# Kernel optimization log

Hardware: AMD Instinct MI355X
Metric: run time of the kernel (lower is better)

The kernel has to match this reference:

```python
import jax, jax.numpy as jnp
import numpy as np
from jax import lax


def setup_inputs() -> dict:
    key = jax.random.key(0)
    k1, k2, k3, k4, k5 = jax.random.split(key, 5)
    B, C_in, H, W = 32768, 3, 14, 14
    C_out, kh, kw = 16, 5, 5
    num_outputs = 1000
    return {
        "feature_map": jax.random.normal(k1, (B, C_in, H, W), dtype=jnp.float32),
        "conv_w": jax.random.normal(k2, (C_out, C_in, kh, kw), dtype=jnp.float32),
        "conv_b": jax.random.normal(k3, (C_out,), dtype=jnp.float32),
        "lin_w": jax.random.normal(k4, (num_outputs, C_out * 5 * 5), dtype=jnp.float32),
        "lin_b": jax.random.normal(k5, (num_outputs,), dtype=jnp.float32),
    }


def reference(feature_map, conv_w, conv_b, lin_w, lin_b):
    # Conv2D: valid cross-correlation, stride 1, no padding (B,Ci,H,W)x(Co,Ci,h,w)->(B,Co,H-h+1,W-w+1)
    y = lax.conv_general_dilated(
        feature_map, conv_w, window_strides=(1, 1), padding="VALID",
        dimension_numbers=("NCHW", "OIHW", "NCHW"))
    y = jax.nn.relu(y + conv_b[None, :, None, None])
    # Non-overlapping 2x2 max pool: (B,C,10,10) -> (B,C,5,5)
    B, C, H, W = y.shape
    y = y.reshape(B, C, H // 2, 2, W // 2, 2).max(axis=(3, 5))
    # Linear head on flattened features (B, C*5*5) -> (B, num_outputs)
    out = y.reshape(B, -1) @ lin_w.T + lin_b
    return out
```

## Files before the change

### kernel.cpp

```cpp
#include <hip/hip_runtime.h>
#include <stdint.h>

#define BTOT 32768
#define NIMG 16
#define KF   416

typedef __attribute__((ext_vector_type(8))) short short8;
typedef __attribute__((ext_vector_type(4))) float floatx4;

__device__ __forceinline__ unsigned short f2bf(float x) {
    union { float f; unsigned int u; } v; v.f = x;
    unsigned int r = v.u + 0x7fffu + ((v.u >> 16) & 1u);
    return (unsigned short)(r >> 16);
}

__global__ __launch_bounds__(256) void conv_pool_kernel(
    const float* __restrict__ fm, const float* __restrict__ cw,
    const float* __restrict__ cb, unsigned short* __restrict__ feat)
{
    __shared__ __align__(16) unsigned short s_img[NIMG * 588];
    __shared__ __align__(16) unsigned short s_out[NIMG * 416];

    const int tid  = threadIdx.x;
    const int b0   = blockIdx.x * NIMG;
    const int lane = tid & 63;
    const int wave = tid >> 6;

    const float4* in4 = (const float4*)(fm + (size_t)b0 * 588);
    for (int idx = tid; idx < NIMG * 147; idx += 256) {
        float4 v = in4[idx];
        unsigned int u0 = (unsigned int)f2bf(v.x) | ((unsigned int)f2bf(v.y) << 16);
        unsigned int u1 = (unsigned int)f2bf(v.z) | ((unsigned int)f2bf(v.w) << 16);
        *(uint2*)&s_img[idx * 4] = make_uint2(u0, u1);
    }
    {
        int img = tid >> 4, k = tid & 15;
        s_out[img * 416 + 400 + k] = 0;
    }

    const int co = lane & 15;
    const int q  = lane >> 4;

    union U8 { unsigned short h[8]; short8 v; };
    U8 bw[3];
    #pragma unroll
    for (int ci = 0; ci < 3; ++ci) {
        #pragma unroll
        for (int j = 0; j < 8; ++j) {
            int t = q * 8 + j;
            bw[ci].h[j] = (t < 25) ? f2bf(cw[co * 75 + ci * 25 + t]) : (unsigned short)0;
        }
    }
    const float bias = cb[co];

    int hoff[8];
    #pragma unroll
    for (int j = 0; j < 8; ++j) {
        int t = q * 8 + j;
        int kh = t / 5;
        hoff[j] = (t < 25) ? (kh * 14 + (t - kh * 5)) : 0;
    }

    const int r  = lane & 15;
    const int qd = r >> 2;
    const int cy = (r >> 1) & 1;
    const int cx = r & 1;

    __syncthreads();

    const unsigned short* sw = s_img + wave * 4 * 588;
    unsigned short* ow = s_out + wave * 4 * 416;

    for (int t = 0; t < 25; ++t) {
        int g   = t * 4 + qd;
        int img = (g * 41) >> 10;
        int q25 = g - img * 25;
        int qy  = (q25 * 13) >> 6;
        int qx  = q25 - qy * 5;
        const unsigned short* p = sw + img * 588 + (qy * 2 + cy) * 14 + (qx * 2 + cx);

        floatx4 acc = {0.f, 0.f, 0.f, 0.f};
        #pragma unroll
        for (int ci = 0; ci < 3; ++ci) {
            union { unsigned int u[4]; short8 v; } a;
            #pragma unroll
            for (int pp = 0; pp < 4; ++pp) {
                unsigned int lo = p[ci * 196 + hoff[2 * pp]];
                unsigned int hi = p[ci * 196 + hoff[2 * pp + 1]];
                a.u[pp] = lo | (hi << 16);
            }
            acc = __builtin_amdgcn_mfma_f32_16x16x32_bf16(a.v, bw[ci].v, acc, 0, 0, 0);
        }

        int gd   = t * 4 + q;
        int imgd = (gd * 41) >> 10;
        int q25d = gd - imgd * 25;
        float m = fmaxf(fmaxf(acc[0], acc[1]), fmaxf(acc[2], acc[3])) + bias;
        ow[imgd * 416 + co * 25 + q25d] = f2bf(fmaxf(m, 0.f));
    }

    __syncthreads();
    const uint4* so4 = (const uint4*)s_out;
    uint4* fo4 = (uint4*)(feat + (size_t)b0 * KF);
    for (int idx = tid; idx < NIMG * 52; idx += 256)
        fo4[idx] = so4[idx];
}

__global__ __launch_bounds__(256) void prep_w_kernel(const float* __restrict__ lw,
                                                     unsigned short* __restrict__ Wb)
{
    int c = blockIdx.x * 256 + threadIdx.x;
    if (c >= 1024 * 52) return;
    int n = c / 52;
    int kc = (c - n * 52) * 8;
    unsigned short v[8];
    #pragma unroll
    for (int j = 0; j < 8; ++j) {
        int k = kc + j;
        float x = (n < 1000 && k < 400) ? lw[n * 400 + k] : 0.f;
        v[j] = f2bf(x);
    }
    *(uint4*)(Wb + (size_t)n * KF + kc) = *(uint4*)v;
}

__global__ __launch_bounds__(256) void gemm_kernel(
    const unsigned short* __restrict__ F, const unsigned short* __restrict__ Wb,
    const float* __restrict__ lb, float* __restrict__ out)
{
    __shared__ __align__(16) unsigned short At[128 * 32];
    __shared__ __align__(16) unsigned short Bt[128 * 32];

    const int tid = threadIdx.x;
    const int bm = blockIdx.x >> 3;
    const int bn = blockIdx.x & 7;
    const int m0 = bm * 128;
    const int n0 = bn * 128;

    const int w = tid >> 6;
    const int lane = tid & 63;
    const int wm = w & 1, wn = w >> 1;
    const int lq = lane >> 4, ln = lane & 15;

    floatx4 zero = {0.f, 0.f, 0.f, 0.f};
    floatx4 acc[4][4];
    #pragma unroll
    for (int i = 0; i < 4; ++i)
        #pragma unroll
        for (int j = 0; j < 4; ++j) acc[i][j] = zero;

    const int srow = w * 16 + (lane >> 2);
    const int skc = (lane & 3) * 8;
    const unsigned short* gA = F + (size_t)(m0 + srow) * KF + skc;
    const unsigned short* gB = Wb + (size_t)(n0 + srow) * KF + skc;

    for (int kb = 0; kb < KF; kb += 32) {
        #pragma unroll
        for (int t = 0; t < 2; ++t) {
            __builtin_amdgcn_global_load_lds(
                (const __attribute__((address_space(1))) void*)(gA + (size_t)(t * 64) * KF + kb),
                (__attribute__((address_space(3))) void*)&At[(w * 16 + t * 64) * 32],
                16, 0, 0);
            __builtin_amdgcn_global_load_lds(
                (const __attribute__((address_space(1))) void*)(gB + (size_t)(t * 64) * KF + kb),
                (__attribute__((address_space(3))) void*)&Bt[(w * 16 + t * 64) * 32],
                16, 0, 0);
        }
        __syncthreads();
        short8 af[4], bf[4];
        #pragma unroll
        for (int i = 0; i < 4; ++i)
            af[i] = *(const short8*)&At[(wm * 64 + i * 16 + ln) * 32 + lq * 8];
        #pragma unroll
        for (int j = 0; j < 4; ++j)
            bf[j] = *(const short8*)&Bt[(wn * 64 + j * 16 + ln) * 32 + lq * 8];
        #pragma unroll
        for (int i = 0; i < 4; ++i)
            #pragma unroll
            for (int j = 0; j < 4; ++j)
                acc[i][j] = __builtin_amdgcn_mfma_f32_16x16x32_bf16(af[i], bf[j], acc[i][j], 0, 0, 0);
        __syncthreads();
    }

    #pragma unroll
    for (int j = 0; j < 4; ++j) {
        int n = n0 + wn * 64 + j * 16 + ln;
        if (n >= 1000) continue;
        float bias = lb[n];
        #pragma unroll
        for (int i = 0; i < 4; ++i) {
            int mb = m0 + wm * 64 + i * 16 + lq * 4;
            #pragma unroll
            for (int rr = 0; rr < 4; ++rr)
                out[(size_t)(mb + rr) * 1000 + n] = acc[i][j][rr] + bias;
        }
    }
}

extern "C" void kernel_launch(void* const* d_in, const int* in_sizes, int n_in,
                              void* d_out, int out_size, void* d_ws, size_t ws_size,
                              hipStream_t stream)
{
    const float* fm = (const float*)d_in[0];
    const float* cw = (const float*)d_in[1];
    const float* cb = (const float*)d_in[2];
    const float* lw = (const float*)d_in[3];
    const float* lb = (const float*)d_in[4];
    float* out = (float*)d_out;

    unsigned short* feat = (unsigned short*)d_ws;
    unsigned short* Wb   = (unsigned short*)d_ws + (size_t)BTOT * KF;

    prep_w_kernel<<<208, 256, 0, stream>>>(lw, Wb);
    conv_pool_kernel<<<BTOT / NIMG, 256, 0, stream>>>(fm, cw, cb, feat);
    gemm_kernel<<<2048, 256, 0, stream>>>(feat, Wb, lb, out);
}
```

Before: 319.4 us.

## Fuse weight prep into conv kernel and restructure conv im2col as row chunks

The linear-weight bf16 conversion moves into extra blocks of the conv kernel, removing one launch. The conv's implicit im2col now packs each 5-tap kernel row into a 32-bit-aligned chunk read with three dword LDS loads plus alignbit. This replaces the 24 scalar 16-bit LDS gathers per MFMA group, at the cost of a fourth, partly zero-padded MFMA per tile. The global-to-LDS staging is also widened to process two float4s per iteration.

```diff
diff --git a/kernel.cpp b/kernel.cpp
--- a/kernel.cpp
+++ b/kernel.cpp
@@ -16,8 +16,26 @@
 
 __global__ __launch_bounds__(256) void conv_pool_kernel(
     const float* __restrict__ fm, const float* __restrict__ cw,
-    const float* __restrict__ cb, unsigned short* __restrict__ feat)
+    const float* __restrict__ cb, unsigned short* __restrict__ feat,
+    const float* __restrict__ lw, unsigned short* __restrict__ Wb)
 {
+    if (blockIdx.x >= BTOT / NIMG) {
+        int c = (blockIdx.x - BTOT / NIMG) * 256 + threadIdx.x;
+        if (c < 1024 * 52) {
+            int n = c / 52;
+            int kc = (c - n * 52) * 8;
+            unsigned short v[8];
+            #pragma unroll
+            for (int j = 0; j < 8; ++j) {
+                int k = kc + j;
+                float x = (n < 1000 && k < 400) ? lw[n * 400 + k] : 0.f;
+                v[j] = f2bf(x);
+            }
+            *(uint4*)(Wb + (size_t)n * KF + kc) = *(uint4*)v;
+        }
+        return;
+    }
+
     __shared__ __align__(16) unsigned short s_img[NIMG * 588];
     __shared__ __align__(16) unsigned short s_out[NIMG * 416];
 
@@ -27,11 +45,14 @@
     const int wave = tid >> 6;
 
     const float4* in4 = (const float4*)(fm + (size_t)b0 * 588);
-    for (int idx = tid; idx < NIMG * 147; idx += 256) {
-        float4 v = in4[idx];
-        unsigned int u0 = (unsigned int)f2bf(v.x) | ((unsigned int)f2bf(v.y) << 16);
-        unsigned int u1 = (unsigned int)f2bf(v.z) | ((unsigned int)f2bf(v.w) << 16);
-        *(uint2*)&s_img[idx * 4] = make_uint2(u0, u1);
+    for (int idx = tid; idx < NIMG * 147 / 2; idx += 256) {
+        float4 v0 = in4[2 * idx], v1 = in4[2 * idx + 1];
+        uint4 u;
+        u.x = (unsigned int)f2bf(v0.x) | ((unsigned int)f2bf(v0.y) << 16);
+        u.y = (unsigned int)f2bf(v0.z) | ((unsigned int)f2bf(v0.w) << 16);
+        u.z = (unsigned int)f2bf(v1.x) | ((unsigned int)f2bf(v1.y) << 16);
+        u.w = (unsigned int)f2bf(v1.z) | ((unsigned int)f2bf(v1.w) << 16);
+        *(uint4*)&s_img[idx * 8] = u;
     }
     {
         int img = tid >> 4, k = tid & 15;
@@ -40,35 +61,31 @@
 
     const int co = lane & 15;
     const int q  = lane >> 4;
-
-    union U8 { unsigned short h[8]; short8 v; };
-    U8 bw[3];
-    #pragma unroll
-    for (int ci = 0; ci < 3; ++ci) {
-        #pragma unroll
-        for (int j = 0; j < 8; ++j) {
-            int t = q * 8 + j;
-            bw[ci].h[j] = (t < 25) ? f2bf(cw[co * 75 + ci * 25 + t]) : (unsigned short)0;
-        }
-    }
-    const float bias = cb[co];
-
-    int hoff[8];
-    #pragma unroll
-    for (int j = 0; j < 8; ++j) {
-        int t = q * 8 + j;
-        int kh = t / 5;
-        hoff[j] = (t < 25) ? (kh * 14 + (t - kh * 5)) : 0;
-    }
-
     const int r  = lane & 15;
     const int qd = r >> 2;
     const int cy = (r >> 1) & 1;
     const int cx = r & 1;
+    const int sh = cx << 4;
+
+    union U8 { unsigned short h[8]; short8 v; };
+    U8 bw[4];
+    int chunkdw[4];
+    #pragma unroll
+    for (int i = 0; i < 4; ++i) {
+        int c = 4 * i + q;
+        int ci = (c < 15) ? (c / 5) : 0;
+        int row = (c < 15) ? (c - ci * 5) : 0;
+        chunkdw[i] = ci * 98 + row * 7;
+        #pragma unroll
+        for (int j = 0; j < 8; ++j)
+            bw[i].h[j] = (c < 15 && j < 5) ? f2bf(cw[co * 75 + ci * 25 + row * 5 + j])
+                                           : (unsigned short)0;
+    }
+    const float bias = cb[co];
 
     __syncthreads();
 
-    const unsigned short* sw = s_img + wave * 4 * 588;
+    const unsigned int* sw32 = (const unsigned int*)s_img + wave * 1176;
     unsigned short* ow = s_out + wave * 4 * 416;
 
     for (int t = 0; t < 25; ++t) {
@@ -77,19 +94,19 @@
         int q25 = g - img * 25;
         int qy  = (q25 * 13) >> 6;
         int qx  = q25 - qy * 5;
-        const unsigned short* p = sw + img * 588 + (qy * 2 + cy) * 14 + (qx * 2 + cx);
+        int wb  = img * 294 + (qy * 2 + cy) * 7 + qx;
 
         floatx4 acc = {0.f, 0.f, 0.f, 0.f};
         #pragma unroll
-        for (int ci = 0; ci < 3; ++ci) {
+        for (int i = 0; i < 4; ++i) {
+            const unsigned int* p = sw32 + wb + chunkdw[i];
+            unsigned int d0 = p[0], d1 = p[1], d2 = p[2];
             union { unsigned int u[4]; short8 v; } a;
-            #pragma unroll
-            for (int pp = 0; pp < 4; ++pp) {
-                unsigned int lo = p[ci * 196 + hoff[2 * pp]];
-                unsigned int hi = p[ci * 196 + hoff[2 * pp + 1]];
-                a.u[pp] = lo | (hi << 16);
-            }
-            acc = __builtin_amdgcn_mfma_f32_16x16x32_bf16(a.v, bw[ci].v, acc, 0, 0, 0);
+            a.u[0] = __builtin_amdgcn_alignbit(d1, d0, sh);
+            a.u[1] = __builtin_amdgcn_alignbit(d2, d1, sh);
+            a.u[2] = __builtin_amdgcn_alignbit(d2, d2, sh);
+            a.u[3] = 0;
+            acc = __builtin_amdgcn_mfma_f32_16x16x32_bf16(a.v, bw[i].v, acc, 0, 0, 0);
         }
 
         int gd   = t * 4 + q;
@@ -104,23 +121,6 @@
     uint4* fo4 = (uint4*)(feat + (size_t)b0 * KF);
     for (int idx = tid; idx < NIMG * 52; idx += 256)
         fo4[idx] = so4[idx];
-}
-
-__global__ __launch_bounds__(256) void prep_w_kernel(const float* __restrict__ lw,
-                                                     unsigned short* __restrict__ Wb)
-{
-    int c = blockIdx.x * 256 + threadIdx.x;
-    if (c >= 1024 * 52) return;
-    int n = c / 52;
-    int kc = (c - n * 52) * 8;
-    unsigned short v[8];
-    #pragma unroll
-    for (int j = 0; j < 8; ++j) {
-        int k = kc + j;
-        float x = (n < 1000 && k < 400) ? lw[n * 400 + k] : 0.f;
-        v[j] = f2bf(x);
-    }
-    *(uint4*)(Wb + (size_t)n * KF + kc) = *(uint4*)v;
 }
 
 __global__ __launch_bounds__(256) void gemm_kernel(
@@ -210,7 +210,6 @@
     unsigned short* feat = (unsigned short*)d_ws;
     unsigned short* Wb   = (unsigned short*)d_ws + (size_t)BTOT * KF;
 
-    prep_w_kernel<<<208, 256, 0, stream>>>(lw, Wb);
-    conv_pool_kernel<<<BTOT / NIMG, 256, 0, stream>>>(fm, cw, cb, feat);
+    conv_pool_kernel<<<BTOT / NIMG + 208, 256, 0, stream>>>(fm, cw, cb, feat, lw, Wb);
     gemm_kernel<<<2048, 256, 0, stream>>>(feat, Wb, lb, out);
 }
```

After: 302.5 us. -5.3%, faster.
